# Kernel tuning notes

Hardware: AMD Instinct MI355X
Metric: run time of the kernel (lower is better)

The kernel has to match this reference:

```python
import jax, jax.numpy as jnp
import numpy as np

Z_DIM = 64
K = 2048
N = 32768


def setup_inputs() -> dict:
    key = jax.random.key(0)
    k1, k2 = jax.random.split(key)
    x = jax.random.normal(k1, (N, Z_DIM), dtype=jnp.float32)
    # init.normal_(locs, std=sqrt(z_dim))
    locs = jax.random.normal(k2, (K, Z_DIM), dtype=jnp.float32) * np.sqrt(Z_DIM)
    logits = jnp.zeros((K,), dtype=jnp.float32)  # maxent buffer
    return {"x": x, "locs": locs, "logits": logits}


def reference(x, locs, logits):
    d = x.shape[-1]
    var = jnp.float32(d)  # scale = sqrt(z_dim) -> variance = z_dim
    # squared distances [N, K] via cdist expansion (avoids [N,K,d] intermediate)
    sq = (
        jnp.sum(x * x, axis=-1, keepdims=True)
        + jnp.sum(locs * locs, axis=-1)[None, :]
        - 2.0 * (x @ locs.T)
    )
    # Independent Normal log prob summed over z_dim
    log_norm_const = d * (0.5 * jnp.log(2.0 * jnp.pi) + 0.5 * jnp.log(var))
    comp_log_prob = -0.5 * sq / var - log_norm_const  # [N, K]
    mix_logits = jax.nn.log_softmax(logits)  # Categorical normalizes logits
    wlp = comp_log_prob + mix_logits  # weighted_log_prob, [N, K]
    log_prob = jax.nn.logsumexp(wlp, axis=-1)  # [N]
    modes = jnp.argmax(wlp, axis=-1)  # assign_modes, [N]
    quantized = locs[modes]  # hard_quantize, [N, z_dim]
    return log_prob, quantized
```

## Files before the change

kernel.cpp:

```cpp
#include <hip/hip_runtime.h>
#include <math.h>

#define N_SAMP 32768
#define K_COMP 2048
#define ZD 64
#define LNC 191.896324792608546f
#define LN2F 0.69314718055994531f
#define INV_LN2 1.44269504088896340f
#define S2C 0.02254211001388974f

typedef __attribute__((ext_vector_type(8))) short short8;
typedef __attribute__((ext_vector_type(4))) float v4f;

#if __has_builtin(__builtin_amdgcn_exp2f)
#define EXP2(x) __builtin_amdgcn_exp2f(x)
#else
#define EXP2(x) exp2f(x)
#endif

__device__ inline unsigned short f2bf(float f) {
    unsigned int u = __float_as_uint(f);
    u += 0x7fffu + ((u >> 16) & 1u);
    return (unsigned short)(u >> 16);
}

__global__ __launch_bounds__(256) void prep_kernel(
    const float* __restrict__ locs, const float* __restrict__ logits,
    float* __restrict__ ck2, float* __restrict__ lse_out,
    char* __restrict__ lf) {
    if (blockIdx.x < 64) {
        int gid = blockIdx.x * 256 + threadIdx.x;
        int k = gid >> 3;
        int dc = gid & 7;
        int T = k >> 4, n = k & 15;

        const float* src = locs + (size_t)k * ZD + dc * 8;
        float4 u0 = *(const float4*)(src);
        float4 u1 = *(const float4*)(src + 4);
        float a[8] = {u0.x, u0.y, u0.z, u0.w, u1.x, u1.y, u1.z, u1.w};

        short8 h;
        float sq = 0.f;
#pragma unroll
        for (int j = 0; j < 8; ++j) {
            h[j] = (short)f2bf(a[j]);
            sq = fmaf(a[j], a[j], sq);
        }
        *(short8*)(lf + (size_t)T * 2048 + (dc >> 2) * 1024 +
                   ((size_t)(n + 16 * (dc & 3))) * 16) = h;

        sq += __shfl_xor(sq, 1);
        sq += __shfl_xor(sq, 2);
        sq += __shfl_xor(sq, 4);
        if (dc == 0) ck2[k] = (logits[k] - sq * (1.0f / 128.0f)) * INV_LN2;
    } else {
        __shared__ float red[4];
        int tid = threadIdx.x;
        int wv = tid >> 6, ln = tid & 63;
        float lm = -INFINITY;
        for (int i = tid; i < K_COMP; i += 256) lm = fmaxf(lm, logits[i]);
#pragma unroll
        for (int d = 1; d < 64; d <<= 1) lm = fmaxf(lm, __shfl_xor(lm, d));
        if (ln == 0) red[wv] = lm;
        __syncthreads();
        float M = fmaxf(fmaxf(red[0], red[1]), fmaxf(red[2], red[3]));
        float ls = 0.f;
        for (int i = tid; i < K_COMP; i += 256) ls += __expf(logits[i] - M);
#pragma unroll
        for (int d = 1; d < 64; d <<= 1) ls += __shfl_xor(ls, d);
        __syncthreads();
        if (ln == 0) red[wv] = ls;
        __syncthreads();
        if (tid == 0) *lse_out = M + __logf(red[0] + red[1] + red[2] + red[3]);
    }
}

__global__ __launch_bounds__(512, 6) void mix_kernel(
    const float* __restrict__ x, const float* __restrict__ locs,
    const char* __restrict__ lf, const float* __restrict__ ck2,
    const float* __restrict__ lse_ptr, float* __restrict__ out) {

    __shared__ float pf[8][32][4];
    __shared__ int   pi[8][32][4];
    __shared__ float xsq_sh[32];
    __shared__ int   cb[3][32];
    __shared__ int   amax_sh[32];

    const int tid  = threadIdx.x;
    const int lane = tid & 63;
    const int kg   = __builtin_amdgcn_readfirstlane(tid >> 6);
    const int n    = lane & 15;
    const int quad = lane >> 4;
    const int sbase = blockIdx.x * 32;

    short8 bh0, bh1, bh2, bh3;
    {
        const float* xp = x + (size_t)(sbase + n) * ZD + quad * 8;
        float4 u0 = *(const float4*)(xp);
        float4 u1 = *(const float4*)(xp + 4);
        float4 u2 = *(const float4*)(xp + 32);
        float4 u3 = *(const float4*)(xp + 36);
        const float* yp = x + (size_t)(sbase + 16 + n) * ZD + quad * 8;
        float4 v0 = *(const float4*)(yp);
        float4 v1 = *(const float4*)(yp + 4);
        float4 v2 = *(const float4*)(yp + 32);
        float4 v3 = *(const float4*)(yp + 36);
        float a[8] = {u0.x, u0.y, u0.z, u0.w, u1.x, u1.y, u1.z, u1.w};
        float b[8] = {u2.x, u2.y, u2.z, u2.w, u3.x, u3.y, u3.z, u3.w};
        float c[8] = {v0.x, v0.y, v0.z, v0.w, v1.x, v1.y, v1.z, v1.w};
        float d[8] = {v2.x, v2.y, v2.z, v2.w, v3.x, v3.y, v3.z, v3.w};
        float pA = 0.f, pB = 0.f;
#pragma unroll
        for (int j = 0; j < 8; ++j) {
            bh0[j] = (short)f2bf(a[j]);
            bh1[j] = (short)f2bf(b[j]);
            bh2[j] = (short)f2bf(c[j]);
            bh3[j] = (short)f2bf(d[j]);
            pA = fmaf(a[j], a[j], pA); pA = fmaf(b[j], b[j], pA);
            pB = fmaf(c[j], c[j], pB); pB = fmaf(d[j], d[j], pB);
        }
        pA += __shfl_xor(pA, 16); pA += __shfl_xor(pA, 32);
        pB += __shfl_xor(pB, 16); pB += __shfl_xor(pB, 32);
        if (kg == 0) {
            if (quad == 0) xsq_sh[n] = pA;
            if (quad == 1) xsq_sh[16 + n] = pB;
        }
    }

    const char* aw = lf + (size_t)(kg * 16) * 2048 + lane * 16;
    const float* ckw = ck2 + kg * 256 + quad * 4;
    const int kb0 = kg * 256 + quad * 4;

    short8 fa[2][2];
    float4 fc[2];

#define LOADA(slot, t) do {                                              \
    const char* _p = aw + (size_t)(t) * 2048;                            \
    fa[slot][0] = *(const short8*)(_p);                                  \
    fa[slot][1] = *(const short8*)(_p + 1024);                           \
    fc[slot] = *(const float4*)(ckw + (t) * 16);                         \
} while (0)

    float sA = 0.f, m1A = -1e30f, m2A = -1e30f, m3A = -1e30f;
    int i1A = 0, i2A = 0, i3A = 0;
    float sB = 0.f, m1B = -1e30f, m2B = -1e30f, m3B = -1e30f;
    int i1B = 0, i2B = 0, i3B = 0;

#define INS(m1, m2, m3, i1, i2, i3, v, kb) do {                          \
    bool c1 = (v) > m1, c2 = (v) > m2, c3 = (v) > m3;                    \
    m3 = c2 ? m2 : (c3 ? (v) : m3);  i3 = c2 ? i2 : (c3 ? (kb) : i3);    \
    m2 = c1 ? m1 : (c2 ? (v) : m2);  i2 = c1 ? i1 : (c2 ? (kb) : i2);    \
    m1 = c1 ? (v) : m1;              i1 = c1 ? (kb) : i1;                \
} while (0)

#define EPI(acc, cc, kb, S, M1, M2, M3, I1, I2, I3) do {                 \
    float w0 = fmaf((acc).x, S2C, (cc).x);                               \
    float w1 = fmaf((acc).y, S2C, (cc).y);                               \
    float w2 = fmaf((acc).z, S2C, (cc).z);                               \
    float w3 = fmaf((acc).w, S2C, (cc).w);                               \
    S += (EXP2(w0) + EXP2(w1)) + (EXP2(w2) + EXP2(w3));                  \
    float v4 = fmaxf(fmaxf(w0, w1), fmaxf(w2, w3));                      \
    INS(M1, M2, M3, I1, I2, I3, v4, kb);                                 \
} while (0)

    LOADA(0, 0);
#pragma unroll
    for (int t = 0; t < 16; ++t) {
        const int slot = t & 1;
        if (t + 1 < 16) LOADA(slot ^ 1, t + 1);

        v4f accA = {0.f, 0.f, 0.f, 0.f};
        v4f accB = {0.f, 0.f, 0.f, 0.f};
        accA = __builtin_amdgcn_mfma_f32_16x16x32_bf16(fa[slot][0], bh0, accA, 0, 0, 0);
        accB = __builtin_amdgcn_mfma_f32_16x16x32_bf16(fa[slot][0], bh2, accB, 0, 0, 0);
        accA = __builtin_amdgcn_mfma_f32_16x16x32_bf16(fa[slot][1], bh1, accA, 0, 0, 0);
        accB = __builtin_amdgcn_mfma_f32_16x16x32_bf16(fa[slot][1], bh3, accB, 0, 0, 0);

        const int kb = kb0 + t * 16;
        float4 cc = fc[slot];
        EPI(accA, cc, kb, sA, m1A, m2A, m3A, i1A, i2A, i3A);
        EPI(accB, cc, kb, sB, m1B, m2B, m3B, i1B, i2B, i3B);
    }

#pragma unroll
    for (int d = 16; d <= 32; d <<= 1) {
        sA += __shfl_xor(sA, d);
        sB += __shfl_xor(sB, d);
        float M1, M2, M3; int I1, I2, I3;
        M1 = __shfl_xor(m1A, d); M2 = __shfl_xor(m2A, d); M3 = __shfl_xor(m3A, d);
        I1 = __shfl_xor(i1A, d); I2 = __shfl_xor(i2A, d); I3 = __shfl_xor(i3A, d);
        INS(m1A, m2A, m3A, i1A, i2A, i3A, M1, I1);
        INS(m1A, m2A, m3A, i1A, i2A, i3A, M2, I2);
        INS(m1A, m2A, m3A, i1A, i2A, i3A, M3, I3);
        M1 = __shfl_xor(m1B, d); M2 = __shfl_xor(m2B, d); M3 = __shfl_xor(m3B, d);
        I1 = __shfl_xor(i1B, d); I2 = __shfl_xor(i2B, d); I3 = __shfl_xor(i3B, d);
        INS(m1B, m2B, m3B, i1B, i2B, i3B, M1, I1);
        INS(m1B, m2B, m3B, i1B, i2B, i3B, M2, I2);
        INS(m1B, m2B, m3B, i1B, i2B, i3B, M3, I3);
    }
    if (quad == 0) {
        pf[kg][n][0] = sA; pf[kg][n][1] = m1A; pf[kg][n][2] = m2A; pf[kg][n][3] = m3A;
        pi[kg][n][0] = i1A; pi[kg][n][1] = i2A; pi[kg][n][2] = i3A;
        pf[kg][16 + n][0] = sB; pf[kg][16 + n][1] = m1B;
        pf[kg][16 + n][2] = m2B; pf[kg][16 + n][3] = m3B;
        pi[kg][16 + n][0] = i1B; pi[kg][16 + n][1] = i2B; pi[kg][16 + n][2] = i3B;
    }
    __syncthreads();

    if (tid < 32) {
        float S = 0.f, m1 = -1e30f, m2 = -1e30f, m3 = -1e30f;
        int i1 = 0, i2 = 0, i3 = 0;
#pragma unroll
        for (int g = 0; g < 8; ++g) {
            S += pf[g][tid][0];
            INS(m1, m2, m3, i1, i2, i3, pf[g][tid][1], pi[g][tid][0]);
            INS(m1, m2, m3, i1, i2, i3, pf[g][tid][2], pi[g][tid][1]);
            INS(m1, m2, m3, i1, i2, i3, pf[g][tid][3], pi[g][tid][2]);
        }
        float bias = -xsq_sh[tid] * (1.0f / 128.0f) - LNC;
        out[sbase + tid] = fmaf(__log2f(S), LN2F, bias - lse_ptr[0]);
        cb[0][tid] = i1; cb[1][tid] = i2; cb[2][tid] = i3;
    }
    __syncthreads();

    if (tid < 256) {
        int s = tid >> 3;
        int j = tid & 7;
        const float4* xrow = (const float4*)(x + (size_t)(sbase + s) * ZD);
        float bestv = -1e30f;
        int bestk = 0x7fffffff;
#pragma unroll
        for (int ci = j; ci < 12; ci += 8) {
            int k = cb[ci >> 2][s] + (ci & 3);
            const float4* lrow = (const float4*)(locs + (size_t)k * ZD);
            float dot = 0.f;
#pragma unroll
            for (int dd = 0; dd < 16; ++dd) {
                float4 xv = xrow[dd];
                float4 lv = lrow[dd];
                dot = fmaf(xv.x, lv.x, dot);
                dot = fmaf(xv.y, lv.y, dot);
                dot = fmaf(xv.z, lv.z, dot);
                dot = fmaf(xv.w, lv.w, dot);
            }
            float v = fmaf(dot, S2C, ck2[k]);
            if (v > bestv || (v == bestv && k < bestk)) { bestv = v; bestk = k; }
        }
#pragma unroll
        for (int d = 1; d <= 4; d <<= 1) {
            float ov = __shfl_xor(bestv, d);
            int   ok = __shfl_xor(bestk, d);
            if (ov > bestv || (ov == bestv && ok < bestk)) { bestv = ov; bestk = ok; }
        }
        if (j == 0) amax_sh[s] = bestk;
    }
    __syncthreads();

    {
        const float4* lq = (const float4*)locs;
        float4* oq = (float4*)(out + N_SAMP + (size_t)sbase * ZD);
        int r = tid >> 4, c = tid & 15;
        oq[tid] = lq[(size_t)amax_sh[r] * (ZD / 4) + c];
    }
#undef LOADA
#undef INS
#undef EPI
}

extern "C" void kernel_launch(void* const* d_in, const int* in_sizes, int n_in,
                              void* d_out, int out_size, void* d_ws, size_t ws_size,
                              hipStream_t stream) {
    const float* x      = (const float*)d_in[0];
    const float* locs   = (const float*)d_in[1];
    const float* logits = (const float*)d_in[2];
    float* out = (float*)d_out;

    float* ck2 = (float*)d_ws;
    float* lse = (float*)((char*)d_ws + 8192);
    char*  lf  = (char*)d_ws + 16384;

    prep_kernel<<<65, 256, 0, stream>>>(locs, logits, ck2, lse, lf);
    mix_kernel<<<N_SAMP / 32, 512, 0, stream>>>(x, locs, lf, ck2, lse, out);
}
```

Baseline: 103.9 us.

## Process 64 samples per block with 4 waves each covering 512 components

Each block now handles 64 samples with 256 threads. Each wave reuses every locs A-fragment across four 16-sample B tiles, so the number of A-fragment global loads per sample falls by half. Each wave covers 512 components over 32 steps with explicit ping-pong double buffering, and the top-3 refinement and gather are reworked to match. The cost is more registers per thread and lower occupancy (launch bounds 256,2), plus half as many blocks.

```diff
diff --git a/kernel.cpp b/kernel.cpp
--- a/kernel.cpp
+++ b/kernel.cpp
@@ -75,61 +75,58 @@
     }
 }
 
-__global__ __launch_bounds__(512, 6) void mix_kernel(
+__global__ __launch_bounds__(256, 2) void mix_kernel(
     const float* __restrict__ x, const float* __restrict__ locs,
     const char* __restrict__ lf, const float* __restrict__ ck2,
     const float* __restrict__ lse_ptr, float* __restrict__ out) {
 
-    __shared__ float pf[8][32][4];
-    __shared__ int   pi[8][32][4];
-    __shared__ float xsq_sh[32];
-    __shared__ int   cb[3][32];
-    __shared__ int   amax_sh[32];
+    __shared__ float pf[4][64][4];
+    __shared__ int   pi[4][64][4];
+    __shared__ float xsq_sh[64];
+    __shared__ int   cb[3][64];
+    __shared__ int   amax_sh[64];
 
     const int tid  = threadIdx.x;
     const int lane = tid & 63;
     const int kg   = __builtin_amdgcn_readfirstlane(tid >> 6);
     const int n    = lane & 15;
     const int quad = lane >> 4;
-    const int sbase = blockIdx.x * 32;
-
-    short8 bh0, bh1, bh2, bh3;
+    const int sbase = blockIdx.x * 64;
+
+    short8 bh[4][2];
     {
-        const float* xp = x + (size_t)(sbase + n) * ZD + quad * 8;
-        float4 u0 = *(const float4*)(xp);
-        float4 u1 = *(const float4*)(xp + 4);
-        float4 u2 = *(const float4*)(xp + 32);
-        float4 u3 = *(const float4*)(xp + 36);
-        const float* yp = x + (size_t)(sbase + 16 + n) * ZD + quad * 8;
-        float4 v0 = *(const float4*)(yp);
-        float4 v1 = *(const float4*)(yp + 4);
-        float4 v2 = *(const float4*)(yp + 32);
-        float4 v3 = *(const float4*)(yp + 36);
-        float a[8] = {u0.x, u0.y, u0.z, u0.w, u1.x, u1.y, u1.z, u1.w};
-        float b[8] = {u2.x, u2.y, u2.z, u2.w, u3.x, u3.y, u3.z, u3.w};
-        float c[8] = {v0.x, v0.y, v0.z, v0.w, v1.x, v1.y, v1.z, v1.w};
-        float d[8] = {v2.x, v2.y, v2.z, v2.w, v3.x, v3.y, v3.z, v3.w};
-        float pA = 0.f, pB = 0.f;
-#pragma unroll
-        for (int j = 0; j < 8; ++j) {
-            bh0[j] = (short)f2bf(a[j]);
-            bh1[j] = (short)f2bf(b[j]);
-            bh2[j] = (short)f2bf(c[j]);
-            bh3[j] = (short)f2bf(d[j]);
-            pA = fmaf(a[j], a[j], pA); pA = fmaf(b[j], b[j], pA);
-            pB = fmaf(c[j], c[j], pB); pB = fmaf(d[j], d[j], pB);
-        }
-        pA += __shfl_xor(pA, 16); pA += __shfl_xor(pA, 32);
-        pB += __shfl_xor(pB, 16); pB += __shfl_xor(pB, 32);
+        float p[4];
+#pragma unroll
+        for (int bt = 0; bt < 4; ++bt) {
+            const float* xp = x + (size_t)(sbase + bt * 16 + n) * ZD + quad * 8;
+            float4 u0 = *(const float4*)(xp);
+            float4 u1 = *(const float4*)(xp + 4);
+            float4 u2 = *(const float4*)(xp + 32);
+            float4 u3 = *(const float4*)(xp + 36);
+            float a[8] = {u0.x, u0.y, u0.z, u0.w, u1.x, u1.y, u1.z, u1.w};
+            float b[8] = {u2.x, u2.y, u2.z, u2.w, u3.x, u3.y, u3.z, u3.w};
+            float pp = 0.f;
+#pragma unroll
+            for (int j = 0; j < 8; ++j) {
+                bh[bt][0][j] = (short)f2bf(a[j]);
+                bh[bt][1][j] = (short)f2bf(b[j]);
+                pp = fmaf(a[j], a[j], pp);
+                pp = fmaf(b[j], b[j], pp);
+            }
+            pp += __shfl_xor(pp, 16);
+            pp += __shfl_xor(pp, 32);
+            p[bt] = pp;
+        }
         if (kg == 0) {
-            if (quad == 0) xsq_sh[n] = pA;
-            if (quad == 1) xsq_sh[16 + n] = pB;
-        }
-    }
-
-    const char* aw = lf + (size_t)(kg * 16) * 2048 + lane * 16;
-    const float* ckw = ck2 + kg * 256 + quad * 4;
-    const int kb0 = kg * 256 + quad * 4;
+            float myp = (quad == 0) ? p[0] : (quad == 1) ? p[1]
+                      : (quad == 2) ? p[2] : p[3];
+            xsq_sh[quad * 16 + n] = myp;
+        }
+    }
+
+    const char* aw = lf + (size_t)(kg * 32) * 2048 + lane * 16;
+    const float* ckw = ck2 + kg * 512 + quad * 4;
+    const int kb0 = kg * 512 + quad * 4;
 
     short8 fa[2][2];
     float4 fc[2];
@@ -141,97 +138,122 @@
     fc[slot] = *(const float4*)(ckw + (t) * 16);                         \
 } while (0)
 
-    float sA = 0.f, m1A = -1e30f, m2A = -1e30f, m3A = -1e30f;
-    int i1A = 0, i2A = 0, i3A = 0;
-    float sB = 0.f, m1B = -1e30f, m2B = -1e30f, m3B = -1e30f;
-    int i1B = 0, i2B = 0, i3B = 0;
-
-#define INS(m1, m2, m3, i1, i2, i3, v, kb) do {                          \
-    bool c1 = (v) > m1, c2 = (v) > m2, c3 = (v) > m3;                    \
-    m3 = c2 ? m2 : (c3 ? (v) : m3);  i3 = c2 ? i2 : (c3 ? (kb) : i3);    \
-    m2 = c1 ? m1 : (c2 ? (v) : m2);  i2 = c1 ? i1 : (c2 ? (kb) : i2);    \
-    m1 = c1 ? (v) : m1;              i1 = c1 ? (kb) : i1;                \
+    float S[4] = {0.f, 0.f, 0.f, 0.f};
+    float m1[4], m2[4], m3[4];
+    int i1[4], i2[4], i3[4];
+#pragma unroll
+    for (int bt = 0; bt < 4; ++bt) {
+        m1[bt] = -1e30f; m2[bt] = -1e30f; m3[bt] = -1e30f;
+        i1[bt] = 0; i2[bt] = 0; i3[bt] = 0;
+    }
+
+#define INS(bt, v, kb) do {                                                       \
+    bool c1 = (v) > m1[bt], c2 = (v) > m2[bt], c3 = (v) > m3[bt];                 \
+    m3[bt] = c2 ? m2[bt] : (c3 ? (v) : m3[bt]);                                   \
+    i3[bt] = c2 ? i2[bt] : (c3 ? (kb) : i3[bt]);                                  \
+    m2[bt] = c1 ? m1[bt] : (c2 ? (v) : m2[bt]);                                   \
+    i2[bt] = c1 ? i1[bt] : (c2 ? (kb) : i2[bt]);                                  \
+    m1[bt] = c1 ? (v) : m1[bt];                                                   \
+    i1[bt] = c1 ? (kb) : i1[bt];                                                  \
 } while (0)
 
-#define EPI(acc, cc, kb, S, M1, M2, M3, I1, I2, I3) do {                 \
-    float w0 = fmaf((acc).x, S2C, (cc).x);                               \
-    float w1 = fmaf((acc).y, S2C, (cc).y);                               \
-    float w2 = fmaf((acc).z, S2C, (cc).z);                               \
-    float w3 = fmaf((acc).w, S2C, (cc).w);                               \
-    S += (EXP2(w0) + EXP2(w1)) + (EXP2(w2) + EXP2(w3));                  \
-    float v4 = fmaxf(fmaxf(w0, w1), fmaxf(w2, w3));                      \
-    INS(M1, M2, M3, I1, I2, I3, v4, kb);                                 \
+#define COMPUTE(slot, t) do {                                                     \
+    v4f acc[4];                                                                   \
+    _Pragma("unroll")                                                             \
+    for (int bt = 0; bt < 4; ++bt) acc[bt] = (v4f){0.f, 0.f, 0.f, 0.f};           \
+    _Pragma("unroll")                                                             \
+    for (int bt = 0; bt < 4; ++bt)                                                \
+        acc[bt] = __builtin_amdgcn_mfma_f32_16x16x32_bf16(                        \
+            fa[slot][0], bh[bt][0], acc[bt], 0, 0, 0);                            \
+    _Pragma("unroll")                                                             \
+    for (int bt = 0; bt < 4; ++bt)                                                \
+        acc[bt] = __builtin_amdgcn_mfma_f32_16x16x32_bf16(                        \
+            fa[slot][1], bh[bt][1], acc[bt], 0, 0, 0);                            \
+    const int kb = kb0 + (t) * 16;                                                \
+    float4 cc = fc[slot];                                                         \
+    _Pragma("unroll")                                                             \
+    for (int bt = 0; bt < 4; ++bt) {                                              \
+        float w0 = fmaf(acc[bt].x, S2C, cc.x);                                    \
+        float w1 = fmaf(acc[bt].y, S2C, cc.y);                                    \
+        float w2 = fmaf(acc[bt].z, S2C, cc.z);                                    \
+        float w3 = fmaf(acc[bt].w, S2C, cc.w);                                    \
+        S[bt] += (EXP2(w0) + EXP2(w1)) + (EXP2(w2) + EXP2(w3));                   \
+        float v4 = fmaxf(fmaxf(w0, w1), fmaxf(w2, w3));                           \
+        INS(bt, v4, kb);                                                          \
+    }                                                                             \
 } while (0)
 
     LOADA(0, 0);
-#pragma unroll
-    for (int t = 0; t < 16; ++t) {
-        const int slot = t & 1;
-        if (t + 1 < 16) LOADA(slot ^ 1, t + 1);
-
-        v4f accA = {0.f, 0.f, 0.f, 0.f};
-        v4f accB = {0.f, 0.f, 0.f, 0.f};
-        accA = __builtin_amdgcn_mfma_f32_16x16x32_bf16(fa[slot][0], bh0, accA, 0, 0, 0);
-        accB = __builtin_amdgcn_mfma_f32_16x16x32_bf16(fa[slot][0], bh2, accB, 0, 0, 0);
-        accA = __builtin_amdgcn_mfma_f32_16x16x32_bf16(fa[slot][1], bh1, accA, 0, 0, 0);
-        accB = __builtin_amdgcn_mfma_f32_16x16x32_bf16(fa[slot][1], bh3, accB, 0, 0, 0);
-
-        const int kb = kb0 + t * 16;
-        float4 cc = fc[slot];
-        EPI(accA, cc, kb, sA, m1A, m2A, m3A, i1A, i2A, i3A);
-        EPI(accB, cc, kb, sB, m1B, m2B, m3B, i1B, i2B, i3B);
-    }
-
-#pragma unroll
-    for (int d = 16; d <= 32; d <<= 1) {
-        sA += __shfl_xor(sA, d);
-        sB += __shfl_xor(sB, d);
-        float M1, M2, M3; int I1, I2, I3;
-        M1 = __shfl_xor(m1A, d); M2 = __shfl_xor(m2A, d); M3 = __shfl_xor(m3A, d);
-        I1 = __shfl_xor(i1A, d); I2 = __shfl_xor(i2A, d); I3 = __shfl_xor(i3A, d);
-        INS(m1A, m2A, m3A, i1A, i2A, i3A, M1, I1);
-        INS(m1A, m2A, m3A, i1A, i2A, i3A, M2, I2);
-        INS(m1A, m2A, m3A, i1A, i2A, i3A, M3, I3);
-        M1 = __shfl_xor(m1B, d); M2 = __shfl_xor(m2B, d); M3 = __shfl_xor(m3B, d);
-        I1 = __shfl_xor(i1B, d); I2 = __shfl_xor(i2B, d); I3 = __shfl_xor(i3B, d);
-        INS(m1B, m2B, m3B, i1B, i2B, i3B, M1, I1);
-        INS(m1B, m2B, m3B, i1B, i2B, i3B, M2, I2);
-        INS(m1B, m2B, m3B, i1B, i2B, i3B, M3, I3);
-    }
-    if (quad == 0) {
-        pf[kg][n][0] = sA; pf[kg][n][1] = m1A; pf[kg][n][2] = m2A; pf[kg][n][3] = m3A;
-        pi[kg][n][0] = i1A; pi[kg][n][1] = i2A; pi[kg][n][2] = i3A;
-        pf[kg][16 + n][0] = sB; pf[kg][16 + n][1] = m1B;
-        pf[kg][16 + n][2] = m2B; pf[kg][16 + n][3] = m3B;
-        pi[kg][16 + n][0] = i1B; pi[kg][16 + n][1] = i2B; pi[kg][16 + n][2] = i3B;
+    for (int t = 0; t < 32; t += 2) {
+        LOADA(1, t + 1);
+        COMPUTE(0, t);
+        int t2 = (t + 2 < 32) ? (t + 2) : 31;
+        LOADA(0, t2);
+        COMPUTE(1, t + 1);
+    }
+
+#pragma unroll
+    for (int bt = 0; bt < 4; ++bt) {
+#pragma unroll
+        for (int d = 16; d <= 32; d <<= 1) {
+            S[bt] += __shfl_xor(S[bt], d);
+            float M1 = __shfl_xor(m1[bt], d), M2 = __shfl_xor(m2[bt], d),
+                  M3 = __shfl_xor(m3[bt], d);
+            int   I1 = __shfl_xor(i1[bt], d), I2 = __shfl_xor(i2[bt], d),
+                  I3 = __shfl_xor(i3[bt], d);
+            INS(bt, M1, I1); INS(bt, M2, I2); INS(bt, M3, I3);
+        }
+    }
+    {
+        int s = quad * 16 + n;
+        float sS  = (quad == 0) ? S[0] : (quad == 1) ? S[1] : (quad == 2) ? S[2] : S[3];
+        float sm1 = (quad == 0) ? m1[0] : (quad == 1) ? m1[1] : (quad == 2) ? m1[2] : m1[3];
+        float sm2 = (quad == 0) ? m2[0] : (quad == 1) ? m2[1] : (quad == 2) ? m2[2] : m2[3];
+        float sm3 = (quad == 0) ? m3[0] : (quad == 1) ? m3[1] : (quad == 2) ? m3[2] : m3[3];
+        int   si1 = (quad == 0) ? i1[0] : (quad == 1) ? i1[1] : (quad == 2) ? i1[2] : i1[3];
+        int   si2 = (quad == 0) ? i2[0] : (quad == 1) ? i2[1] : (quad == 2) ? i2[2] : i2[3];
+        int   si3 = (quad == 0) ? i3[0] : (quad == 1) ? i3[1] : (quad == 2) ? i3[2] : i3[3];
+        pf[kg][s][0] = sS;  pf[kg][s][1] = sm1; pf[kg][s][2] = sm2; pf[kg][s][3] = sm3;
+        pi[kg][s][0] = si1; pi[kg][s][1] = si2; pi[kg][s][2] = si3;
     }
     __syncthreads();
 
-    if (tid < 32) {
-        float S = 0.f, m1 = -1e30f, m2 = -1e30f, m3 = -1e30f;
-        int i1 = 0, i2 = 0, i3 = 0;
-#pragma unroll
-        for (int g = 0; g < 8; ++g) {
-            S += pf[g][tid][0];
-            INS(m1, m2, m3, i1, i2, i3, pf[g][tid][1], pi[g][tid][0]);
-            INS(m1, m2, m3, i1, i2, i3, pf[g][tid][2], pi[g][tid][1]);
-            INS(m1, m2, m3, i1, i2, i3, pf[g][tid][3], pi[g][tid][2]);
+    if (tid < 64) {
+        float Sx = 0.f, M1 = -1e30f, M2 = -1e30f, M3 = -1e30f;
+        int I1 = 0, I2 = 0, I3 = 0;
+#pragma unroll
+        for (int g = 0; g < 4; ++g) {
+            Sx += pf[g][tid][0];
+            float a1 = pf[g][tid][1], a2 = pf[g][tid][2], a3 = pf[g][tid][3];
+            int   b1 = pi[g][tid][0], b2 = pi[g][tid][1], b3 = pi[g][tid][2];
+            bool c1 = a1 > M1, c2 = a1 > M2, c3 = a1 > M3;
+            M3 = c2 ? M2 : (c3 ? a1 : M3);  I3 = c2 ? I2 : (c3 ? b1 : I3);
+            M2 = c1 ? M1 : (c2 ? a1 : M2);  I2 = c1 ? I1 : (c2 ? b1 : I2);
+            M1 = c1 ? a1 : M1;              I1 = c1 ? b1 : I1;
+            c1 = a2 > M1; c2 = a2 > M2; c3 = a2 > M3;
+            M3 = c2 ? M2 : (c3 ? a2 : M3);  I3 = c2 ? I2 : (c3 ? b2 : I3);
+            M2 = c1 ? M1 : (c2 ? a2 : M2);  I2 = c1 ? I1 : (c2 ? b2 : I2);
+            M1 = c1 ? a2 : M1;              I1 = c1 ? b2 : I1;
+            c1 = a3 > M1; c2 = a3 > M2; c3 = a3 > M3;
+            M3 = c2 ? M2 : (c3 ? a3 : M3);  I3 = c2 ? I2 : (c3 ? b3 : I3);
+            M2 = c1 ? M1 : (c2 ? a3 : M2);  I2 = c1 ? I1 : (c2 ? b3 : I2);
+            M1 = c1 ? a3 : M1;              I1 = c1 ? b3 : I1;
         }
         float bias = -xsq_sh[tid] * (1.0f / 128.0f) - LNC;
-        out[sbase + tid] = fmaf(__log2f(S), LN2F, bias - lse_ptr[0]);
-        cb[0][tid] = i1; cb[1][tid] = i2; cb[2][tid] = i3;
+        out[sbase + tid] = fmaf(__log2f(Sx), LN2F, bias - lse_ptr[0]);
+        cb[0][tid] = I1; cb[1][tid] = I2; cb[2][tid] = I3;
     }
     __syncthreads();
 
-    if (tid < 256) {
-        int s = tid >> 3;
-        int j = tid & 7;
+    {
+        int s = tid >> 2;
+        int j = tid & 3;
         const float4* xrow = (const float4*)(x + (size_t)(sbase + s) * ZD);
         float bestv = -1e30f;
         int bestk = 0x7fffffff;
 #pragma unroll
-        for (int ci = j; ci < 12; ci += 8) {
-            int k = cb[ci >> 2][s] + (ci & 3);
+        for (int ci = 0; ci < 3; ++ci) {
+            int k = cb[ci][s] + j;
             const float4* lrow = (const float4*)(locs + (size_t)k * ZD);
             float dot = 0.f;
 #pragma unroll
@@ -247,7 +269,7 @@
             if (v > bestv || (v == bestv && k < bestk)) { bestv = v; bestk = k; }
         }
 #pragma unroll
-        for (int d = 1; d <= 4; d <<= 1) {
+        for (int d = 1; d <= 2; d <<= 1) {
             float ov = __shfl_xor(bestv, d);
             int   ok = __shfl_xor(bestk, d);
             if (ov > bestv || (ov == bestv && ok < bestk)) { bestv = ov; bestk = ok; }
@@ -256,15 +278,16 @@
     }
     __syncthreads();
 
-    {
-        const float4* lq = (const float4*)locs;
-        float4* oq = (float4*)(out + N_SAMP + (size_t)sbase * ZD);
-        int r = tid >> 4, c = tid & 15;
-        oq[tid] = lq[(size_t)amax_sh[r] * (ZD / 4) + c];
+    const float4* lq = (const float4*)locs;
+    float4* oq = (float4*)(out + N_SAMP + (size_t)sbase * ZD);
+#pragma unroll
+    for (int i = tid; i < 64 * (ZD / 4); i += 256) {
+        int r = i >> 4, c = i & 15;
+        oq[i] = lq[(size_t)amax_sh[r] * (ZD / 4) + c];
     }
 #undef LOADA
 #undef INS
-#undef EPI
+#undef COMPUTE
 }
 
 extern "C" void kernel_launch(void* const* d_in, const int* in_sizes, int n_in,
@@ -280,5 +303,5 @@
     char*  lf  = (char*)d_ws + 16384;
 
     prep_kernel<<<65, 256, 0, stream>>>(locs, logits, ck2, lse, lf);
-    mix_kernel<<<N_SAMP / 32, 512, 0, stream>>>(x, locs, lf, ck2, lse, out);
+    mix_kernel<<<N_SAMP / 64, 256, 0, stream>>>(x, locs, lf, ck2, lse, out);
 }
```

Measured after the change: 106.8 us. 2.7% more time.
